# Kernel tuning notes

Hardware: AMD Instinct MI355X
Metric: run time of the kernel (lower is better)

The kernel has to match this reference:

```python
import jax, jax.numpy as jnp
import numpy as np

BETA = 4.0  # temperature of soft cluster assignment in filling loss


def _pairwise_sq_dist(a, b):
    # a: [N,D], b: [K,D] -> [N,K] squared euclidean distances
    return (jnp.sum(a * a, -1, keepdims=True)
            - 2.0 * (a @ b.T)
            + jnp.sum(b * b, -1)[None, :])


def setup_inputs() -> dict:
    key = jax.random.key(0)
    k1, k2, k3, k4 = jax.random.split(key, 4)
    N, D, K = 131072, 64, 16
    x = jax.random.normal(k1, (N, D), jnp.float32)
    cluster_centers = jax.random.normal(k2, (K, D), jnp.float32)
    target = jax.random.normal(k3, (N, D), jnp.float32)
    ft = jax.random.uniform(k4, (K,), jnp.float32)
    filling_target = ft / ft.sum()
    # prediction = kmeans assignment of the fixed target set (computed once, constant)
    prediction = jnp.argmin(_pairwise_sq_dist(target, cluster_centers), axis=-1)
    return {"x": x, "cluster_centers": cluster_centers,
            "filling_target": filling_target, "target": target,
            "prediction": prediction}


def reference(x, cluster_centers, filling_target, target, prediction):
    N, D = x.shape
    Nt = target.shape[0]
    K = cluster_centers.shape[0]
    BIG = jnp.finfo(x.dtype).max  # padding value that sorts to the end

    d2 = _pairwise_sq_dist(x, cluster_centers)  # [N,K]

    # --- cluster filling MSE: soft assignment fractions vs filling_target ---
    soft = jax.nn.softmax(-BETA * d2, axis=-1)          # [N,K]
    filling = soft.mean(axis=0)                          # [K]
    loss_fil = jnp.mean((filling - filling_target) ** 2)

    # --- per-cluster sorted (per-dimension 1D) Wasserstein distance ---
    pred_x = jax.lax.stop_gradient(jnp.argmin(d2, axis=-1))  # kmeans_predict(x).detach()
    L = min(N, Nt)  # static upper bound on per-cluster min_size
    rows = jnp.arange(L)

    loss_med = jnp.zeros((), x.dtype)
    for k in range(K):  # fixed structural loop over clusters
        mx = pred_x == k
        mt = prediction == k
        m = jnp.minimum(mx.sum(), mt.sum())  # min_size (dynamic value, static shapes)
        # keep only the FIRST m members (original order), as x[in_cluster][:m]
        keep_x = mx & ((jnp.cumsum(mx) - 1) < m)
        keep_t = mt & ((jnp.cumsum(mt) - 1) < m)
        # mask out non-members with BIG so they sort to the bottom, sort per dim
        xs = jnp.sort(jnp.where(keep_x[:, None], x, BIG), axis=0)[:L]       # [L,D]
        ts = jnp.sort(jnp.where(keep_t[:, None], target, BIG), axis=0)[:L]  # [L,D]
        valid = (rows < m)[:, None]                                          # [L,1]
        diff = jnp.where(valid, jnp.abs(xs - ts), 0.0)
        # mean(|sort(x) - sort(y)|) over the m x D selected elements
        denom = (m * D).astype(x.dtype)
        loss_med = loss_med + jnp.where(m > 0, diff.sum() / denom, 0.0)

    return loss_fil + loss_med
```

## Files before the change

### kernel.cpp

```cpp
#include <hip/hip_runtime.h>
#include <hip/hip_cooperative_groups.h>
#include <stdint.h>

namespace cg = cooperative_groups;

#define N_ROWS 131072
#define DIMS 64
#define KCL 16
#define BETA 4.0f
#define NBLK 512
#define CHUNK 16384
#define STH 1024
#define SEG_STRIDE 263168
#define VOFF (1u<<21)

typedef unsigned long long u64;
typedef unsigned int u32;

__device__ __forceinline__ u32 enc_f(float f) {
  u32 u = __float_as_uint(f);
  return (u & 0x80000000u) ? ~u : (u | 0x80000000u);
}
__device__ __forceinline__ float dec_f(u32 e) {
  u32 u = (e & 0x80000000u) ? (e & 0x7FFFFFFFu) : ~e;
  return __uint_as_float(u);
}
__device__ __forceinline__ u32 U4(u32 u) { return u ^ ((u >> 3) & 7u); }

#define CS(a,b,dd) { u32 _mn = min(a,b), _mx = max(a,b); a = (dd)?_mn:_mx; b = (dd)?_mx:_mn; }
#define CSV(A,B,D) { CS(A.x,B.x,D) CS(A.y,B.y,D) CS(A.z,B.z,D) CS(A.w,B.w,D) }

#define M16G(a,b,c,d,e,f,g,h,i2,j2,k2,l,m,n,o,p,D) \
  CS(a,i2,D) CS(b,j2,D) CS(c,k2,D) CS(d,l,D) CS(e,m,D) CS(f,n,D) CS(g,o,D) CS(h,p,D) \
  CS(a,e,D)  CS(b,f,D)  CS(c,g,D)  CS(d,h,D) CS(i2,m,D) CS(j2,n,D) CS(k2,o,D) CS(l,p,D) \
  CS(a,c,D)  CS(b,d,D)  CS(e,g,D)  CS(f,h,D) CS(i2,k2,D) CS(j2,l,D) CS(m,o,D) CS(n,p,D) \
  CS(a,b,D)  CS(c,d,D)  CS(e,f,D)  CS(g,h,D) CS(i2,j2,D) CS(k2,l,D) CS(m,n,D) CS(o,p,D)

#define SORT16G(a,b,c,d,e,f,g,h,i2,j2,k2,l,m,n,o,p,D) \
  CS(a,b,D) CS(c,d,!(D)) CS(e,f,D) CS(g,h,!(D)) CS(i2,j2,D) CS(k2,l,!(D)) CS(m,n,D) CS(o,p,!(D)) \
  CS(a,c,D) CS(b,d,D) CS(e,g,!(D)) CS(f,h,!(D)) CS(i2,k2,D) CS(j2,l,D) CS(m,o,!(D)) CS(n,p,!(D)) \
  CS(a,b,D) CS(c,d,D) CS(e,f,!(D)) CS(g,h,!(D)) CS(i2,j2,D) CS(k2,l,D) CS(m,n,!(D)) CS(o,p,!(D)) \
  CS(a,e,D) CS(b,f,D) CS(c,g,D) CS(d,h,D) CS(i2,m,!(D)) CS(j2,n,!(D)) CS(k2,o,!(D)) CS(l,p,!(D)) \
  CS(a,c,D) CS(b,d,D) CS(e,g,D) CS(f,h,D) CS(i2,k2,!(D)) CS(j2,l,!(D)) CS(m,o,!(D)) CS(n,p,!(D)) \
  CS(a,b,D) CS(c,d,D) CS(e,f,D) CS(g,h,D) CS(i2,j2,!(D)) CS(k2,l,!(D)) CS(m,n,!(D)) CS(o,p,!(D)) \
  M16G(a,b,c,d,e,f,g,h,i2,j2,k2,l,m,n,o,p,D)

#define MERGE16F(D) M16G(r0,r1,r2,r3,r4,r5,r6,r7,r8,r9,r10,r11,r12,r13,r14,r15,D)
#define SORT16F(D)  SORT16G(r0,r1,r2,r3,r4,r5,r6,r7,r8,r9,r10,r11,r12,r13,r14,r15,D)

#define LOADTILE16(src) \
  { uint4 _a0=src[U4(ub+0)],_a1=src[U4(ub+1)],_a2=src[U4(ub+2)],_a3=src[U4(ub+3)]; \
    r0=_a0.x;r1=_a0.y;r2=_a0.z;r3=_a0.w; r4=_a1.x;r5=_a1.y;r6=_a1.z;r7=_a1.w; \
    r8=_a2.x;r9=_a2.y;r10=_a2.z;r11=_a2.w; r12=_a3.x;r13=_a3.y;r14=_a3.z;r15=_a3.w; }

#define STORETILE16(dst) \
  { dst[U4(ub+0)]=make_uint4(r0,r1,r2,r3);   dst[U4(ub+1)]=make_uint4(r4,r5,r6,r7); \
    dst[U4(ub+2)]=make_uint4(r8,r9,r10,r11); dst[U4(ub+3)]=make_uint4(r12,r13,r14,r15); }

__device__ __forceinline__ void wave_tail(uint4* lds4, u32 RU, u32 Lw, u32 gbase,
                                          u32 k, u32 jtop, u32 lane)
{
  u32 j = jtop;
  while (j >= 32u) {
    u32 ud = j >> 3;
    if (lane < (Lw >> 4)) {
      u32 bu = RU + (((lane & ~(ud - 1u)) << 2) | (lane & (ud - 1u)));
      bool up = (((gbase + (bu << 2)) & k) == 0u);
      uint4 A0 = lds4[U4(bu)],           A1 = lds4[U4(bu + ud)],
            A2 = lds4[U4(bu + 2u * ud)], A3 = lds4[U4(bu + 3u * ud)];
      CSV(A0,A2,up) CSV(A1,A3,up)
      CSV(A0,A1,up) CSV(A2,A3,up)
      lds4[U4(bu)] = A0;           lds4[U4(bu + ud)] = A1;
      lds4[U4(bu + 2u * ud)] = A2; lds4[U4(bu + 3u * ud)] = A3;
    }
    j >>= 2;
  }
  if (j == 16u) {
    u32 total = Lw >> 3;
    for (u32 inst = lane; inst < total; inst += 64u) {
      u32 bu = RU + (((inst & ~3u) << 1) | (inst & 3u));
      bool up = (((gbase + (bu << 2)) & k) == 0u);
      uint4 A = lds4[U4(bu)], B = lds4[U4(bu + 4u)];
      CSV(A,B,up)
      lds4[U4(bu)] = A; lds4[U4(bu + 4u)] = B;
    }
  }
}

__device__ __forceinline__ void cross1(uint4* lds4, u32 Wn, u32 gb, u32 k, u32 jtop, u32 tid)
{
  u32 ud = jtop >> 2;
  u32 total = Wn >> 3;
  for (u32 inst = tid; inst < total; inst += STH) {
    u32 bu = ((inst & ~(ud - 1u)) << 1) | (inst & (ud - 1u));
    bool up = (((gb + (bu << 2)) & k) == 0u);
    uint4 A = lds4[U4(bu)], B = lds4[U4(bu + ud)];
    CSV(A,B,up)
    lds4[U4(bu)] = A; lds4[U4(bu + ud)] = B;
  }
}
__device__ __forceinline__ void cross2(uint4* lds4, u32 Wn, u32 gb, u32 k, u32 jtop, u32 tid)
{
  u32 ud = jtop >> 3;
  u32 total = Wn >> 4;
  for (u32 inst = tid; inst < total; inst += STH) {
    u32 bu = ((inst & ~(ud - 1u)) << 2) | (inst & (ud - 1u));
    bool up = (((gb + (bu << 2)) & k) == 0u);
    uint4 A0 = lds4[U4(bu)],            A1 = lds4[U4(bu + ud)],
          A2 = lds4[U4(bu + 2u * ud)],  A3 = lds4[U4(bu + 3u * ud)];
    CSV(A0,A2,up) CSV(A1,A3,up)
    CSV(A0,A1,up) CSV(A2,A3,up)
    lds4[U4(bu)] = A0;           lds4[U4(bu + ud)] = A1;
    lds4[U4(bu + 2u * ud)] = A2; lds4[U4(bu + 3u * ud)] = A3;
  }
}
__device__ __forceinline__ void cross3(uint4* lds4, u32 Wn, u32 gb, u32 k, u32 jtop, u32 tid)
{
  u32 ud = jtop >> 4;
  u32 total = Wn >> 5;
  for (u32 inst = tid; inst < total; inst += STH) {
    u32 bu = ((inst & ~(ud - 1u)) << 3) | (inst & (ud - 1u));
    bool up = (((gb + (bu << 2)) & k) == 0u);
    uint4 A0 = lds4[U4(bu)],            A1 = lds4[U4(bu + ud)],
          A2 = lds4[U4(bu + 2u * ud)],  A3 = lds4[U4(bu + 3u * ud)],
          A4 = lds4[U4(bu + 4u * ud)],  A5 = lds4[U4(bu + 5u * ud)],
          A6 = lds4[U4(bu + 6u * ud)],  A7 = lds4[U4(bu + 7u * ud)];
    CSV(A0,A4,up) CSV(A1,A5,up) CSV(A2,A6,up) CSV(A3,A7,up)
    CSV(A0,A2,up) CSV(A1,A3,up) CSV(A4,A6,up) CSV(A5,A7,up)
    CSV(A0,A1,up) CSV(A2,A3,up) CSV(A4,A5,up) CSV(A6,A7,up)
    lds4[U4(bu)] = A0;           lds4[U4(bu + ud)] = A1;
    lds4[U4(bu + 2u * ud)] = A2; lds4[U4(bu + 3u * ud)] = A3;
    lds4[U4(bu + 4u * ud)] = A4; lds4[U4(bu + 5u * ud)] = A5;
    lds4[U4(bu + 6u * ud)] = A6; lds4[U4(bu + 7u * ud)] = A7;
  }
}

__global__ __launch_bounds__(256) void k_assign(
    const float* __restrict__ x, const float* __restrict__ centers,
    const int* __restrict__ predT, int* __restrict__ predX,
    float* __restrict__ fill_sum, u32* __restrict__ histX, u32* __restrict__ histT)
{
  __shared__ float c[KCL][DIMS];
  __shared__ float cn[KCL];
  __shared__ float fs[KCL];
  __shared__ u32 hx[KCL], ht[KCL];
  int tid = threadIdx.x;
  for (int t = tid; t < KCL * DIMS; t += 256) c[t / DIMS][t % DIMS] = centers[t];
  if (tid < KCL) { fs[tid] = 0.f; hx[tid] = 0; ht[tid] = 0; }
  __syncthreads();
  if (tid < KCL) {
    float s = 0.f;
    for (int d = 0; d < DIMS; ++d) s += c[tid][d] * c[tid][d];
    cn[tid] = s;
  }
  __syncthreads();
  int i = blockIdx.x * 256 + tid;
  const float4* xr = (const float4*)(x + (size_t)i * DIMS);
  float dot[KCL];
#pragma unroll
  for (int k = 0; k < KCL; ++k) dot[k] = 0.f;
  for (int t = 0; t < DIMS / 4; ++t) {
    float4 v = xr[t];
#pragma unroll
    for (int k = 0; k < KCL; ++k)
      dot[k] += v.x * c[k][4 * t] + v.y * c[k][4 * t + 1] + v.z * c[k][4 * t + 2] + v.w * c[k][4 * t + 3];
  }
  float sc[KCL];
  float smin = 3.0e38f; int kmin = 0;
#pragma unroll
  for (int k = 0; k < KCL; ++k) {
    sc[k] = cn[k] - 2.f * dot[k];
    if (sc[k] < smin) { smin = sc[k]; kmin = k; }
  }
  float e[KCL]; float esum = 0.f;
#pragma unroll
  for (int k = 0; k < KCL; ++k) { e[k] = expf(-BETA * (sc[k] - smin)); esum += e[k]; }
  float inv = 1.f / esum;
#pragma unroll
  for (int k = 0; k < KCL; ++k) atomicAdd(&fs[k], e[k] * inv);
  predX[i] = kmin;
  atomicAdd(&hx[kmin], 1u);
  atomicAdd(&ht[predT[i]], 1u);
  __syncthreads();
  if (tid < KCL) {
    histX[blockIdx.x * KCL + tid] = hx[tid];
    histT[blockIdx.x * KCL + tid] = ht[tid];
    atomicAdd(&fill_sum[tid], fs[tid]);
  }
}

__global__ __launch_bounds__(512) void k_scan(
    const u32* __restrict__ histX, const u32* __restrict__ histT,
    u32* __restrict__ baseX, u32* __restrict__ baseT,
    const float* __restrict__ fill_sum, const float* __restrict__ ftarget,
    int* __restrict__ m_out, float* __restrict__ w_out,
    int* __restrict__ p_out, int* __restrict__ pOff_out, int* __restrict__ mOff_out,
    int* __restrict__ nlo_out, float* __restrict__ loss_fil)
{
  __shared__ u32 part[2][KCL][17];
  __shared__ u32 tot[2][KCL];
  __shared__ float sq[KCL];
  __shared__ int sp[KCL];
  __shared__ int smv[KCL];
  int tid = threadIdx.x;
  int side = tid >> 8;
  int rem = tid & 255;
  int c = rem >> 4;
  int sub = rem & 15;
  const u32* hist = side ? histT : histX;
  u32* base = side ? baseT : baseX;
  int b0 = sub * 32;
  u32 s = 0;
  for (int b = b0; b < b0 + 32; ++b) s += hist[b * KCL + c];
  part[side][c][sub] = s;
  __syncthreads();
  if (sub == 0) {
    u32 run = 0;
    for (int t = 0; t < 16; ++t) { u32 v = part[side][c][t]; part[side][c][t] = run; run += v; }
    tot[side][c] = run;
  }
  __syncthreads();
  u32 run = part[side][c][sub];
  for (int b = b0; b < b0 + 32; ++b) { base[b * KCL + c] = run; run += hist[b * KCL + c]; }
  if (tid < KCL) {
    int m = min((int)tot[0][tid], (int)tot[1][tid]);
    m_out[tid] = m;
    smv[tid] = m;
    w_out[tid] = (m > 0) ? 1.f / ((float)m * (float)DIMS) : 0.f;
    int pp = 32;
    while (pp < m) pp <<= 1;
    sp[tid] = pp;
    p_out[tid] = pp;
    int nlo = 0;
    if (pp > CHUNK) {
      int nch = pp / CHUNK;
      for (int j = 1; j < nch; j += 2) {
        int v = m - j * CHUNK;
        if (v < 0) v = 0;
        if (v > CHUNK) v = CHUNK;
        nlo += CHUNK - v;
      }
    }
    nlo_out[tid] = nlo;
    float d = fill_sum[tid] / (float)N_ROWS - ftarget[tid];
    sq[tid] = d * d;
  }
  __syncthreads();
  if (tid == 0) {
    float s2 = 0.f;
    int acc = 0, macc = 0;
    for (int k = 0; k < KCL; ++k) {
      s2 += sq[k];
      pOff_out[k] = acc;
      acc += sp[k];
      mOff_out[k] = macc;
      macc += smv[k];
    }
    pOff_out[KCL] = acc;
    mOff_out[KCL] = macc;
    *loss_fil = s2 / (float)KCL;
  }
}

__global__ __launch_bounds__(256) void k_rank(
    const int* __restrict__ predX, const int* __restrict__ predT,
    const u32* __restrict__ baseX, const u32* __restrict__ baseT,
    const int* __restrict__ mG, const int* __restrict__ mOffG,
    int* __restrict__ idxX, int* __restrict__ idxT)
{
  __shared__ int wcX[4][KCL], wcT[4][KCL];
  __shared__ int smo[KCL], sm2[KCL];
  int tid = threadIdx.x;
  int lane = tid & 63, wave = tid >> 6;
  if (tid < KCL) { smo[tid] = mOffG[tid]; sm2[tid] = mG[tid]; }
  int i = blockIdx.x * 256 + tid;
  int kx = predX[i], kt = predT[i];
  u64 below = (1ull << lane) - 1ull;
  int lrX = 0, lrT = 0;
  for (int cc = 0; cc < KCL; ++cc) {
    u64 mx = __ballot(kx == cc);
    u64 mt = __ballot(kt == cc);
    if (kx == cc) lrX = __popcll(mx & below);
    if (kt == cc) lrT = __popcll(mt & below);
    if (lane == 0) { wcX[wave][cc] = __popcll(mx); wcT[wave][cc] = __popcll(mt); }
  }
  __syncthreads();
  int wbX = 0, wbT = 0;
  for (int w2 = 0; w2 < wave; ++w2) { wbX += wcX[w2][kx]; wbT += wcT[w2][kt]; }
  int rX = (int)baseX[blockIdx.x * KCL + kx] + wbX + lrX;
  int rT = (int)baseT[blockIdx.x * KCL + kt] + wbT + lrT;
  if (rX < sm2[kx]) idxX[smo[kx] + rX] = i;
  if (rT < sm2[kt]) idxT[smo[kt] + rT] = i;
}

__global__ __launch_bounds__(256) void k_gather(
    const float* __restrict__ x, const float* __restrict__ tgt,
    const int* __restrict__ idxX, const int* __restrict__ idxT,
    const int* __restrict__ pOffG, const int* __restrict__ mOffG,
    const int* __restrict__ mG, const int* __restrict__ pG,
    u32* __restrict__ valX, u32* __restrict__ valT, int d0, int Dbc)
{
  __shared__ int spOff[KCL + 1];
  __shared__ int smo[KCL], sm2[KCL], sp2[KCL];
  int tid = threadIdx.x;
  if (tid <= KCL) spOff[tid] = pOffG[tid];
  if (tid < KCL) { smo[tid] = mOffG[tid]; sm2[tid] = mG[tid]; sp2[tid] = pG[tid]; }
  __syncthreads();
  int pos = blockIdx.x * 256 + tid;
  if (pos >= spOff[KCL]) return;
  int c = 0;
#pragma unroll
  for (int cc = 1; cc < KCL; ++cc) c += (pos >= spOff[cc]) ? 1 : 0;
  int rel = pos - spOff[c];
  u32* dx = valX + pos;
  u32* dt = valT + pos;
  if (rel < sm2[c]) {
    int w = smo[c] + rel;
    int iX = idxX[w], iT = idxT[w];
    if ((Dbc & 3) == 0) {
      const float4* xr = (const float4*)(x + (size_t)iX * DIMS + d0);
      const float4* tr = (const float4*)(tgt + (size_t)iT * DIMS + d0);
      for (int q = 0; q < (Dbc >> 2); ++q) {
        float4 a = xr[q];
        float4 b = tr[q];
        size_t base = (size_t)(4 * q) * SEG_STRIDE;
        dx[base]                  = enc_f(a.x);
        dx[base + SEG_STRIDE]     = enc_f(a.y);
        dx[base + 2 * (size_t)SEG_STRIDE] = enc_f(a.z);
        dx[base + 3 * (size_t)SEG_STRIDE] = enc_f(a.w);
        dt[base]                  = enc_f(b.x);
        dt[base + SEG_STRIDE]     = enc_f(b.y);
        dt[base + 2 * (size_t)SEG_STRIDE] = enc_f(b.z);
        dt[base + 3 * (size_t)SEG_STRIDE] = enc_f(b.w);
      }
    } else {
      const float* xr = x + (size_t)iX * DIMS + d0;
      const float* tr = tgt + (size_t)iT * DIMS + d0;
      for (int d = 0; d < Dbc; ++d) {
        dx[(size_t)d * SEG_STRIDE] = enc_f(xr[d]);
        dt[(size_t)d * SEG_STRIDE] = enc_f(tr[d]);
      }
    }
  } else {
    u32 pv = (sp2[c] > CHUNK && ((rel >> 14) & 1)) ? 0u : 0xFFFFFFFFu;
    for (int d = 0; d < Dbc; ++d) {
      dx[(size_t)d * SEG_STRIDE] = pv;
      dt[(size_t)d * SEG_STRIDE] = pv;
    }
  }
}

__global__ __launch_bounds__(STH, 8) void k_sort(
    u32* __restrict__ vbase, const int* __restrict__ pG, const int* __restrict__ pOffG,
    const int* __restrict__ mG)
{
  __shared__ __align__(16) u32 lds[CHUNK];
  uint4* lds4 = (uint4*)lds;
  int t = blockIdx.x, c = -1, sub = 0, acc = 0;
  for (int cc = 0; cc < KCL; ++cc) {
    int pc0 = pG[cc];
    int nc = (pc0 > CHUNK) ? (pc0 / CHUNK) : 1;
    if (t < acc + nc) { c = cc; sub = t - acc; break; }
    acc += nc;
  }
  if (c < 0) return;
  int pc = pG[c];
  u32 CH = (u32)min(pc, CHUNK);
  u32 gb = (u32)sub * (u32)CHUNK;
  int v = mG[c] - (int)gb;
  if (v > (int)CH) v = (int)CH;
  if (v <= 0) return;
  u32 W = 32u;
  while (W < (u32)v) W <<= 1;
  if (W > CH) W = CH;
  bool desc = (pc > CHUNK) && (sub & 1);
  u32 inv = desc ? 0xFFFFFFFFu : 0u;
  u32* seg = vbase + (size_t)blockIdx.y * SEG_STRIDE + pOffG[c] + gb;
  uint4* gp4 = (uint4*)seg;
  u32 tid = threadIdx.x;
  u32 lane = tid & 63u;
  u32 wv = tid >> 6;
  u32 ub = tid << 2;
  u32 bas = tid << 4;
  bool act = (bas < W);
  u32 RU = wv << 8;
  u32 runBase = wv << 10;
  bool wact = (runBase < W);
  u32 Lw = W - runBase; if (Lw > 1024u) Lw = 1024u;
  u32 r0,r1,r2,r3,r4,r5,r6,r7,r8,r9,r10,r11,r12,r13,r14,r15;

  if (act) {
    uint4 a0 = gp4[ub + 0], a1 = gp4[ub + 1], a2 = gp4[ub + 2], a3 = gp4[ub + 3];
    r0 = a0.x^inv; r1 = a0.y^inv; r2  = a0.z^inv; r3  = a0.w^inv;
    r4 = a1.x^inv; r5 = a1.y^inv; r6  = a1.z^inv; r7  = a1.w^inv;
    r8 = a2.x^inv; r9 = a2.y^inv; r10 = a2.z^inv; r11 = a2.w^inv;
    r12 = a3.x^inv; r13 = a3.y^inv; r14 = a3.z^inv; r15 = a3.w^inv;
    bool D = ((bas & 16u) == 0u);
    SORT16F(D);
    STORETILE16(lds4);
  }
  if (wact) {
    for (u32 k = 32u; k <= Lw; k <<= 1) {
      wave_tail(lds4, RU, Lw, 0u, k, k >> 1, lane);
      if (act) {
        LOADTILE16(lds4);
        bool D = ((bas & k) == 0u);
        MERGE16F(D);
        STORETILE16(lds4);
      }
    }
  }

  if (W >= 2048u) {
    __syncthreads();
    for (u32 k = 2048u; k <= W; k <<= 1) {
      u32 jt = k >> 1;
      if (jt >= 8192u) {
        cross3(lds4, W, 0u, k, 8192u, tid);
        __syncthreads();
        cross1(lds4, W, 0u, k, 1024u, tid);
        __syncthreads();
      } else if (jt == 4096u) {
        cross3(lds4, W, 0u, k, 4096u, tid);
        __syncthreads();
      } else if (jt == 2048u) {
        cross2(lds4, W, 0u, k, 2048u, tid);
        __syncthreads();
      } else {
        cross1(lds4, W, 0u, k, 1024u, tid);
        __syncthreads();
      }
      if (wact) {
        wave_tail(lds4, RU, Lw, 0u, k, 512u, lane);
        if (act) {
          LOADTILE16(lds4);
          bool D = ((bas & k) == 0u);
          MERGE16F(D);
          STORETILE16(lds4);
        }
      }
      if (k < W) __syncthreads();
    }
  }

  __syncthreads();
  for (u32 uu = tid; (uu << 2) < W; uu += STH) {
    uint4 q = lds4[U4(uu)];
    q.x ^= inv; q.y ^= inv; q.z ^= inv; q.w ^= inv;
    gp4[uu] = q;
  }
}

__global__ __launch_bounds__(STH) void k_gbig(
    u32* __restrict__ vbase, const int* __restrict__ pG,
    const int* __restrict__ pOffG, int nplanes)
{
  __shared__ __align__(16) u32 lds[CHUNK];
  uint4* lds4 = (uint4*)lds;
  int p[KCL], pO[KCL];
  int pmax = 0;
#pragma unroll
  for (int c = 0; c < KCL; ++c) {
    p[c] = pG[c]; pO[c] = pOffG[c];
    pmax = max(pmax, p[c]);
  }
  if (pmax <= CHUNK) return;
  cg::grid_group grid = cg::this_grid();
  u32 tid = threadIdx.x;
  u32 lane = tid & 63u, wv = tid >> 6, RU = wv << 8, ub = tid << 2, bas = tid << 4;

  for (int kk = 2 * CHUNK; kk <= N_ROWS; kk <<= 1) {
    if (pmax < kk) break;
    for (int j = kk >> 1; j >= CHUNK; j >>= 1) {
      int pb[KCL]; int tot = 0;
#pragma unroll
      for (int c = 0; c < KCL; ++c) { pb[c] = tot; if (p[c] >= kk) tot += p[c] >> 3; }
      long total = (long)tot * nplanes;
      long gthr = (long)gridDim.x * STH;
      for (long g = (long)blockIdx.x * STH + tid; g < total; g += gthr) {
        int plane = (int)(g / tot);
        int u4i = (int)(g % tot);
        int c = 0;
#pragma unroll
        for (int cc = 1; cc < KCL; ++cc) c += (u4i >= pb[cc]) ? 1 : 0;
        int u = (u4i - pb[c]) << 2;
        int i = ((u & ~(j - 1)) << 1) | (u & (j - 1));
        bool up = ((i & kk) == 0);
        u32* s2 = vbase + (size_t)plane * SEG_STRIDE + pO[c];
        uint4 A = *(const uint4*)(s2 + i);
        uint4 B = *(const uint4*)(s2 + i + j);
        CS(A.x, B.x, up) CS(A.y, B.y, up) CS(A.z, B.z, up) CS(A.w, B.w, up)
        *(uint4*)(s2 + i) = A;
        *(uint4*)(s2 + i + j) = B;
      }
      grid.sync();
    }
    int cb[KCL]; int nch = 0;
#pragma unroll
    for (int c = 0; c < KCL; ++c) { cb[c] = nch; if (p[c] >= kk) nch += p[c] / CHUNK; }
    int totc = nch * nplanes;
    for (int item = blockIdx.x; item < totc; item += gridDim.x) {
      int plane = item / nch;
      int ch = item % nch;
      int c = 0;
#pragma unroll
      for (int cc = 1; cc < KCL; ++cc) c += (ch >= cb[cc]) ? 1 : 0;
      int sub = ch - cb[c];
      u32 gb = (u32)sub * (u32)CHUNK;
      u32* seg = vbase + (size_t)plane * SEG_STRIDE + pO[c] + gb;
      uint4* gp4 = (uint4*)seg;
      for (u32 uu = tid; uu < CHUNK / 4; uu += STH) lds4[U4(uu)] = gp4[uu];
      __syncthreads();
      cross3(lds4, (u32)CHUNK, gb, (u32)kk, 8192u, tid);
      __syncthreads();
      cross1(lds4, (u32)CHUNK, gb, (u32)kk, 1024u, tid);
      __syncthreads();
      wave_tail(lds4, RU, 1024u, gb, (u32)kk, 512u, lane);
      {
        u32 r0,r1,r2,r3,r4,r5,r6,r7,r8,r9,r10,r11,r12,r13,r14,r15;
        LOADTILE16(lds4);
        bool up = (((gb + bas) & (u32)kk) == 0u);
        MERGE16F(up);
        STORETILE16(lds4);
      }
      __syncthreads();
      for (u32 uu = tid; uu < CHUNK / 4; uu += STH) gp4[uu] = lds4[U4(uu)];
      __syncthreads();
    }
    grid.sync();
  }
}

__global__ __launch_bounds__(256) void k_reduce(
    const u32* __restrict__ valX, const u32* __restrict__ valT,
    const int* __restrict__ pOffG, const int* __restrict__ mOffG,
    const int* __restrict__ nloG,
    const float* __restrict__ wG, float* __restrict__ lossAcc)
{
  __shared__ int spOff[KCL];
  __shared__ int smo[KCL + 1];
  __shared__ int snlo[KCL];
  __shared__ float swt[KCL];
  __shared__ float red[256];
  int tid = threadIdx.x;
  if (tid <= KCL) smo[tid] = mOffG[tid];
  if (tid < KCL) { spOff[tid] = pOffG[tid]; snlo[tid] = nloG[tid]; swt[tid] = wG[tid]; }
  __syncthreads();
  int d = blockIdx.y;
  const u32* vx = valX + (size_t)d * SEG_STRIDE;
  const u32* vt = valT + (size_t)d * SEG_STRIDE;
  int M = smo[KCL];
  float s = 0.f;
  for (int w = blockIdx.x * 256 + tid; w < M; w += gridDim.x * 256) {
    int c = 0;
#pragma unroll
    for (int cc = 1; cc < KCL; ++cc) c += (w >= smo[cc]) ? 1 : 0;
    int pos = spOff[c] + snlo[c] + (w - smo[c]);
    float a = dec_f(vx[pos]), b = dec_f(vt[pos]);
    s += fabsf(a - b) * swt[c];
  }
  red[tid] = s;
  __syncthreads();
  for (int st = 128; st > 0; st >>= 1) {
    if (tid < st) red[tid] += red[tid + st];
    __syncthreads();
  }
  if (tid == 0) atomicAdd(lossAcc, red[0]);
}

__global__ void k_final(const float* __restrict__ lossAcc, const float* __restrict__ loss_fil,
                        float* __restrict__ out)
{
  out[0] = *lossAcc + *loss_fil;
}

extern "C" void kernel_launch(void* const* d_in, const int* in_sizes, int n_in,
                              void* d_out, int out_size, void* d_ws, size_t ws_size,
                              hipStream_t stream)
{
  const float* x       = (const float*)d_in[0];
  const float* centers = (const float*)d_in[1];
  const float* ftarget = (const float*)d_in[2];
  const float* tgt     = (const float*)d_in[3];
  const int*   predT   = (const int*)d_in[4];
  float* out = (float*)d_out;

  char* ws = (char*)d_ws;
  float* fill_sum = (float*)(ws + 0);
  float* lossAcc  = (float*)(ws + 64);
  float* loss_fil = (float*)(ws + 68);
  int*   m_buf    = (int*)(ws + 128);
  float* w_buf    = (float*)(ws + 192);
  int*   p_buf    = (int*)(ws + 256);
  int*   pOff     = (int*)(ws + 320);
  int*   mOff     = (int*)(ws + 400);
  u32* histX = (u32*)(ws + 512);
  u32* histT = (u32*)(ws + 512 + 32768);
  u32* baseX = (u32*)(ws + 512 + 65536);
  u32* baseT = (u32*)(ws + 512 + 98304);
  int* predX = (int*)(ws + 131584);
  int* idxX  = (int*)(ws + 655872);
  int* idxT  = (int*)(ws + 1180160);
  int* nlo_buf = (int*)(ws + 1704448);
  u32* vbase = (u32*)(ws + VOFF);

  size_t avail_elems = (ws_size > VOFF) ? ((ws_size - VOFF) / 4) : 0;
  int Db = (int)(avail_elems / (2ull * SEG_STRIDE));
  if (Db > DIMS) Db = DIMS;
  if (Db >= 4) Db &= ~3;
  if (Db < 1) Db = 1;

  hipMemsetAsync(ws, 0, 128, stream);
  k_assign<<<NBLK, 256, 0, stream>>>(x, centers, predT, predX, fill_sum, histX, histT);
  k_scan<<<1, 512, 0, stream>>>(histX, histT, baseX, baseT, fill_sum, ftarget,
                                m_buf, w_buf, p_buf, pOff, mOff, nlo_buf, loss_fil);
  k_rank<<<NBLK, 256, 0, stream>>>(predX, predT, baseX, baseT, m_buf, mOff, idxX, idxT);

  for (int d0 = 0; d0 < DIMS; d0 += Db) {
    int Dbc = (Db < DIMS - d0) ? Db : (DIMS - d0);
    u32* valX = vbase;
    u32* valT = vbase + (size_t)Dbc * SEG_STRIDE;
    k_gather<<<1028, 256, 0, stream>>>(x, tgt, idxX, idxT, pOff, mOff, m_buf, p_buf,
                                       valX, valT, d0, Dbc);
    k_sort<<<dim3(26, 2 * Dbc), STH, 0, stream>>>(vbase, p_buf, pOff, m_buf);
    {
      u32* vb = vbase;
      const int* pb = p_buf;
      const int* po = pOff;
      int np = 2 * Dbc;
      void* gargs[] = { (void*)&vb, (void*)&pb, (void*)&po, (void*)&np };
      hipLaunchCooperativeKernel((const void*)k_gbig, dim3(256), dim3(STH),
                                 gargs, 0, stream);
    }
    k_reduce<<<dim3(32, Dbc), 256, 0, stream>>>(valX, valT, pOff, mOff, nlo_buf,
                                                w_buf, lossAcc);
  }
  k_final<<<1, 1, 0, stream>>>(lossAcc, loss_fil, out);
}
```

Measured before the change: 738.9 us.

## Replace cooperative grid-synced big-merge kernel with per-cluster-plane blocks

The large bitonic merge stages for clusters bigger than one LDS chunk now run with one workgroup per (cluster, plane) pair, using block-level barriers instead of a cooperative launch with grid-wide syncs. This removes grid.sync overhead and the cooperative launch. In exchange, each large segment is processed by a single block serially, which can limit parallelism when few clusters are large and work is imbalanced.

Result: slower. 1.076 ms (+45.7%).

```diff
diff --git a/kernel.cpp b/kernel.cpp
--- a/kernel.cpp
+++ b/kernel.cpp
@@ -1,8 +1,5 @@
 #include <hip/hip_runtime.h>
-#include <hip/hip_cooperative_groups.h>
 #include <stdint.h>
-
-namespace cg = cooperative_groups;
 
 #define N_ROWS 131072
 #define DIMS 64
@@ -452,63 +449,36 @@
 }
 
 __global__ __launch_bounds__(STH) void k_gbig(
-    u32* __restrict__ vbase, const int* __restrict__ pG,
-    const int* __restrict__ pOffG, int nplanes)
-{
+    u32* __restrict__ vbase, const int* __restrict__ pG, const int* __restrict__ pOffG)
+{
+  int c = blockIdx.x;
+  int pc = pG[c];
+  if (pc <= CHUNK) return;
   __shared__ __align__(16) u32 lds[CHUNK];
   uint4* lds4 = (uint4*)lds;
-  int p[KCL], pO[KCL];
-  int pmax = 0;
-#pragma unroll
-  for (int c = 0; c < KCL; ++c) {
-    p[c] = pG[c]; pO[c] = pOffG[c];
-    pmax = max(pmax, p[c]);
-  }
-  if (pmax <= CHUNK) return;
-  cg::grid_group grid = cg::this_grid();
+  u32* seg = vbase + (size_t)blockIdx.y * SEG_STRIDE + pOffG[c];
   u32 tid = threadIdx.x;
   u32 lane = tid & 63u, wv = tid >> 6, RU = wv << 8, ub = tid << 2, bas = tid << 4;
 
-  for (int kk = 2 * CHUNK; kk <= N_ROWS; kk <<= 1) {
-    if (pmax < kk) break;
+  for (int kk = 2 * CHUNK; kk <= pc; kk <<= 1) {
     for (int j = kk >> 1; j >= CHUNK; j >>= 1) {
-      int pb[KCL]; int tot = 0;
-#pragma unroll
-      for (int c = 0; c < KCL; ++c) { pb[c] = tot; if (p[c] >= kk) tot += p[c] >> 3; }
-      long total = (long)tot * nplanes;
-      long gthr = (long)gridDim.x * STH;
-      for (long g = (long)blockIdx.x * STH + tid; g < total; g += gthr) {
-        int plane = (int)(g / tot);
-        int u4i = (int)(g % tot);
-        int c = 0;
-#pragma unroll
-        for (int cc = 1; cc < KCL; ++cc) c += (u4i >= pb[cc]) ? 1 : 0;
-        int u = (u4i - pb[c]) << 2;
+      int pairs4 = pc >> 3;
+      for (int u4i = tid; u4i < pairs4; u4i += STH) {
+        int u = u4i << 2;
         int i = ((u & ~(j - 1)) << 1) | (u & (j - 1));
         bool up = ((i & kk) == 0);
-        u32* s2 = vbase + (size_t)plane * SEG_STRIDE + pO[c];
-        uint4 A = *(const uint4*)(s2 + i);
-        uint4 B = *(const uint4*)(s2 + i + j);
+        uint4 A = *(const uint4*)(seg + i);
+        uint4 B = *(const uint4*)(seg + i + j);
         CS(A.x, B.x, up) CS(A.y, B.y, up) CS(A.z, B.z, up) CS(A.w, B.w, up)
-        *(uint4*)(s2 + i) = A;
-        *(uint4*)(s2 + i + j) = B;
-      }
-      grid.sync();
-    }
-    int cb[KCL]; int nch = 0;
-#pragma unroll
-    for (int c = 0; c < KCL; ++c) { cb[c] = nch; if (p[c] >= kk) nch += p[c] / CHUNK; }
-    int totc = nch * nplanes;
-    for (int item = blockIdx.x; item < totc; item += gridDim.x) {
-      int plane = item / nch;
-      int ch = item % nch;
-      int c = 0;
-#pragma unroll
-      for (int cc = 1; cc < KCL; ++cc) c += (ch >= cb[cc]) ? 1 : 0;
-      int sub = ch - cb[c];
+        *(uint4*)(seg + i) = A;
+        *(uint4*)(seg + i + j) = B;
+      }
+      __syncthreads();
+    }
+    int nch = pc / CHUNK;
+    for (int sub = 0; sub < nch; ++sub) {
       u32 gb = (u32)sub * (u32)CHUNK;
-      u32* seg = vbase + (size_t)plane * SEG_STRIDE + pO[c] + gb;
-      uint4* gp4 = (uint4*)seg;
+      uint4* gp4 = (uint4*)(seg + gb);
       for (u32 uu = tid; uu < CHUNK / 4; uu += STH) lds4[U4(uu)] = gp4[uu];
       __syncthreads();
       cross3(lds4, (u32)CHUNK, gb, (u32)kk, 8192u, tid);
@@ -527,7 +497,6 @@
       for (u32 uu = tid; uu < CHUNK / 4; uu += STH) gp4[uu] = lds4[U4(uu)];
       __syncthreads();
     }
-    grid.sync();
   }
 }
 
@@ -623,15 +592,7 @@
     k_gather<<<1028, 256, 0, stream>>>(x, tgt, idxX, idxT, pOff, mOff, m_buf, p_buf,
                                        valX, valT, d0, Dbc);
     k_sort<<<dim3(26, 2 * Dbc), STH, 0, stream>>>(vbase, p_buf, pOff, m_buf);
-    {
-      u32* vb = vbase;
-      const int* pb = p_buf;
-      const int* po = pOff;
-      int np = 2 * Dbc;
-      void* gargs[] = { (void*)&vb, (void*)&pb, (void*)&po, (void*)&np };
-      hipLaunchCooperativeKernel((const void*)k_gbig, dim3(256), dim3(STH),
-                                 gargs, 0, stream);
-    }
+    k_gbig<<<dim3(KCL, 2 * Dbc), STH, 0, stream>>>(vbase, p_buf, pOff);
     k_reduce<<<dim3(32, Dbc), 256, 0, stream>>>(valX, valT, pOff, mOff, nlo_buf,
                                                 w_buf, lossAcc);
   }
```
